# Optimization experiments

Hardware: AMD Instinct MI355X
Metric: run time of the kernel (lower is better)

## Reference

```python
import jax, jax.numpy as jnp
import numpy as np
from jax import lax

N_GROUPS = 128
EPS = 1e-5


def _instance_norm(x):
    # x: [B, C, H, W]; per-sample per-channel normalization over spatial dims
    mean = jnp.mean(x, axis=(2, 3), keepdims=True)
    var = jnp.mean(jnp.square(x - mean), axis=(2, 3), keepdims=True)
    return (x - mean) * lax.rsqrt(var + EPS)


def _reflect_pad(x, p):
    return jnp.pad(x, ((0, 0), (0, 0), (p, p), (p, p)), mode='reflect')


def _conv(x, w, groups):
    # x: [N, Cin, H, W], w: [Cout, Cin/groups, kh, kw], VALID padding
    return lax.conv_general_dilated(
        x, w, window_strides=(1, 1), padding='VALID',
        dimension_numbers=('NCHW', 'OIHW', 'NCHW'),
        feature_group_count=groups)


def _forward_single(xi, ws, wp, b):
    # xi: [1, C, H, W]; ws: [C_mid, C/G, k, k]; wp: [C_pw, C_mid/G, 1, 1]; b: [C_pw]
    k = ws.shape[-1]
    p = (k - 1) // 2  # k=3 -> ceil/floor both 1
    y = _conv(_reflect_pad(xi, p), ws, N_GROUPS)
    y = _conv(y, wp, N_GROUPS) + b[None, :, None, None]
    return y


def setup_inputs() -> dict:
    key = jax.random.key(0)
    ks = jax.random.split(key, 6)
    B, C, H, W = 4, 512, 128, 128
    x = jax.random.normal(ks[0], (B, C, H, W), dtype=jnp.float32)
    w_spatial = jax.random.normal(ks[1], (B, 512, 4, 3, 3), dtype=jnp.float32) * 0.05
    w_pointwise = jax.random.normal(ks[2], (B, 128, 4, 1, 1), dtype=jnp.float32) * 0.05
    bias = jax.random.normal(ks[3], (B, 128), dtype=jnp.float32) * 0.05
    conv_w = jax.random.normal(ks[4], (512, 512, 3, 3), dtype=jnp.float32) * 0.02
    conv_b = jax.random.normal(ks[5], (512,), dtype=jnp.float32) * 0.02
    return {"x": x, "w_spatial": w_spatial, "w_pointwise": w_pointwise,
            "bias": bias, "conv_w": conv_w, "conv_b": conv_b}


def reference(x, w_spatial, w_pointwise, bias, conv_w, conv_b):
    B, C, H, W = x.shape
    x = _instance_norm(x)
    # per-sample grouped spatial + pointwise conv, vmapped over batch
    ys = jax.vmap(_forward_single)(x[:, None], w_spatial, w_pointwise, bias)
    # ys: [B, 1, C_pw, H, W] -> concat along channel dim as in torch.cat(dim=1)
    ys = ys.reshape(1, B * ys.shape[2], H, W)
    # final standard conv, reflect padding (1,1), kernel 3
    out = _conv(_reflect_pad(ys, 1), conv_w, 1) + conv_b[None, :, None, None]
    return out
```

## Files before the change

### kernel.cpp

```cpp
#include <hip/hip_runtime.h>
#include <hip/hip_bf16.h>


typedef unsigned short u16;
typedef __attribute__((ext_vector_type(8))) short bf16x8;
typedef __attribute__((ext_vector_type(4))) float f32x4;

#define HW 16384
#define NBC 2048

__device__ __forceinline__ int refl(int i) {
    return i < 0 ? -i : (i > 127 ? 254 - i : i);
}

__device__ __forceinline__ u16 f2bf(float f) {
    union { float f; unsigned u; } x; x.f = f;
    unsigned r = x.u + 0x7fffu + ((x.u >> 16) & 1u);
    return (u16)(r >> 16);
}

__global__ __launch_bounds__(256) void stats_kernel(
        const float* __restrict__ x, float* __restrict__ mean,
        float* __restrict__ rstd) {
    int bc = blockIdx.x;
    const float4* p4 = (const float4*)(x + (size_t)bc * HW);
    float s = 0.f, ss = 0.f;
    for (int i = threadIdx.x; i < HW / 4; i += 256) {
        float4 v = p4[i];
        s  += v.x + v.y + v.z + v.w;
        ss += v.x * v.x + v.y * v.y + v.z * v.z + v.w * v.w;
    }
    for (int o = 32; o >= 1; o >>= 1) {
        s  += __shfl_down(s, o);
        ss += __shfl_down(ss, o);
    }
    __shared__ float sm[4], sm2[4];
    int wid = threadIdx.x >> 6, lane = threadIdx.x & 63;
    if (lane == 0) { sm[wid] = s; sm2[wid] = ss; }
    __syncthreads();
    if (threadIdx.x == 0) {
        float S = sm[0] + sm[1] + sm[2] + sm[3];
        float SS = sm2[0] + sm2[1] + sm2[2] + sm2[3];
        float m = S * (1.f / HW);
        float var = SS * (1.f / HW) - m * m;
        mean[bc] = m;
        rstd[bc] = rsqrtf(var + 1e-5f);
    }
}

__global__ __launch_bounds__(256) void weff_kernel(
        const float* __restrict__ wsp, const float* __restrict__ wpw,
        float* __restrict__ we) {
    int idx = blockIdx.x * 256 + threadIdx.x;
    if (idx >= 4 * 128 * 4 * 9) return;
    int k = idx % 9;
    int c = (idx / 9) & 3;
    int g = (idx / 36) & 127;
    int b = idx / 4608;
    float acc = 0.f;
#pragma unroll
    for (int m = 0; m < 4; ++m) {
        acc += wpw[(b * 128 + g) * 4 + m] *
               wsp[(((size_t)b * 512 + g * 4 + m) * 4 + c) * 9 + k];
    }
    we[idx] = acc;
}

__global__ __launch_bounds__(256) void midconv_kernel(
        const float* __restrict__ x, const float* __restrict__ mean,
        const float* __restrict__ rstd, const float* __restrict__ we,
        const float* __restrict__ bias, float* __restrict__ ys) {
    int bg = blockIdx.z;
    int b = bg >> 7, g = bg & 127;
    int x0 = blockIdx.x * 16, y0 = blockIdx.y * 16;
    __shared__ float tile[4][18][18];
    int t = threadIdx.x;
    for (int idx = t; idx < 4 * 18 * 18; idx += 256) {
        int c = idx / 324;
        int rem = idx - c * 324;
        int r = rem / 18, col = rem - r * 18;
        int ch = (b << 9) + (g << 2) + c;
        int gh = refl(y0 + r - 1), gw = refl(x0 + col - 1);
        float m = mean[ch], rs = rstd[ch];
        tile[c][r][col] = (x[((size_t)ch << 14) + (gh << 7) + gw] - m) * rs;
    }
    __syncthreads();
    int lx = t & 15, ly = t >> 4;
    const float* w = we + (size_t)bg * 36;
    float acc = bias[bg];
#pragma unroll
    for (int c = 0; c < 4; ++c)
#pragma unroll
        for (int kh = 0; kh < 3; ++kh)
#pragma unroll
            for (int kw = 0; kw < 3; ++kw)
                acc += w[c * 9 + kh * 3 + kw] * tile[c][ly + kh][lx + kw];
    ys[((size_t)bg << 14) + ((size_t)(y0 + ly) << 7) + (x0 + lx)] = acc;
}

__global__ __launch_bounds__(256) void transpose_ys(
        const float* __restrict__ ys, u16* __restrict__ ysT) {
    __shared__ u16 tile[64][72];
    int t = threadIdx.x;
    int pix0 = blockIdx.x * 64, ci0 = blockIdx.y * 64;
    for (int i = t; i < 64 * 16; i += 256) {
        int ci = i >> 4, px = (i & 15) * 4;
        float4 v = *(const float4*)&ys[(size_t)(ci0 + ci) * HW + pix0 + px];
        tile[ci][px + 0] = f2bf(v.x);
        tile[ci][px + 1] = f2bf(v.y);
        tile[ci][px + 2] = f2bf(v.z);
        tile[ci][px + 3] = f2bf(v.w);
    }
    __syncthreads();
    for (int i = t; i < 512; i += 256) {
        int px = i >> 3, c8 = i & 7;
        bf16x8 v;
#pragma unroll
        for (int j = 0; j < 8; ++j) v[j] = (short)tile[c8 * 8 + j][px];
        *(bf16x8*)&ysT[(size_t)(pix0 + px) * 512 + ci0 + c8 * 8] = v;
    }
}

__global__ __launch_bounds__(256) void wpack_kernel(
        const float* __restrict__ cw, u16* __restrict__ wT) {
    int idx = blockIdx.x * 256 + threadIdx.x;
    if (idx >= 9 * 512 * 512) return;
    int ci = idx & 511;
    int co = (idx >> 9) & 511;
    int tap = idx >> 18;
    wT[idx] = f2bf(cw[(size_t)co * 4608 + ci * 9 + tap]);
}

__device__ __forceinline__ void load_lds16(const u16* g, u16* l) {
    __builtin_amdgcn_global_load_lds(
        (const __attribute__((address_space(1))) unsigned int*)g,
        (__attribute__((address_space(3))) unsigned int*)l, 16, 0, 0);
}

__global__ __launch_bounds__(256, 2) void finalconv_mfma(
        const u16* __restrict__ ysT, const u16* __restrict__ wT,
        const float* __restrict__ cb, float* __restrict__ out) {
    __shared__ u16 lds_ys[528 * 32];
    __shared__ u16 lds_wt[576 * 32];
    int t = threadIdx.x;
    int w = t >> 6, l = t & 63;
    int m = l & 15, q = l >> 4;
    int co0 = blockIdx.x * 64;
    int y0 = blockIdx.y * 2;
    int tr = w >> 1, xw = (w & 1) * 64;

    f32x4 acc[4][4];
#pragma unroll
    for (int i = 0; i < 4; ++i)
#pragma unroll
        for (int j = 0; j < 4; ++j) acc[i][j] = (f32x4){0.f, 0.f, 0.f, 0.f};

    for (int ci0 = 0; ci0 < 512; ci0 += 32) {
        __syncthreads();
        for (int i = w; i < 69; i += 4) {
            if (i < 33) {
                int s = i * 64 + l;
                int p = s >> 2, c = s & 3;
                int pc = p > 519 ? 519 : p;
                int hr = (pc * 1009) >> 17;
                int hc = pc - hr * 130;
                int gy = refl(y0 + hr - 1), gx = refl(hc - 1);
                int ci8 = c ^ ((p >> 1) & 3);
                const u16* src = ysT + (size_t)((gy << 7) + gx) * 512 + ci0 + ci8 * 8;
                load_lds16(src, &lds_ys[i * 512]);
            } else {
                int k = i - 33;
                int s = k * 64 + l;
                int row = s >> 2, c = s & 3;
                int tap = row >> 6, co_l = row & 63;
                int ci8 = c ^ ((co_l >> 1) & 3);
                const u16* src = wT + (size_t)((tap << 9) + co0 + co_l) * 512 + ci0 + ci8 * 8;
                load_lds16(src, &lds_wt[k * 512]);
            }
        }
        __syncthreads();
#pragma unroll
        for (int tap = 0; tap < 9; ++tap) {
            const int dyi = tap / 3, dxi = tap % 3;
            bf16x8 a[4], b[4];
#pragma unroll
            for (int i = 0; i < 4; ++i) {
                int co_l = i * 16 + m;
                int ch = q ^ ((co_l >> 1) & 3);
                a[i] = *(const bf16x8*)&lds_wt[(tap * 64 + co_l) * 32 + ch * 8];
            }
#pragma unroll
            for (int j = 0; j < 4; ++j) {
                int xx = xw + j * 16 + m;
                int p = (tr + dyi) * 130 + xx + dxi;
                int ch = q ^ ((p >> 1) & 3);
                b[j] = *(const bf16x8*)&lds_ys[p * 32 + ch * 8];
            }
#pragma unroll
            for (int i = 0; i < 4; ++i)
#pragma unroll
                for (int j = 0; j < 4; ++j)
                    acc[i][j] = __builtin_amdgcn_mfma_f32_16x16x32_bf16(
                        a[i], b[j], acc[i][j], 0, 0, 0);
        }
    }
    int gyo = y0 + tr;
#pragma unroll
    for (int i = 0; i < 4; ++i) {
        int cob = co0 + i * 16 + q * 4;
#pragma unroll
        for (int j = 0; j < 4; ++j) {
            int xx = xw + j * 16 + m;
            float* o = out + (size_t)cob * HW + (gyo << 7) + xx;
#pragma unroll
            for (int r = 0; r < 4; ++r)
                o[(size_t)r * HW] = acc[i][j][r] + cb[cob + r];
        }
    }
}

extern "C" void kernel_launch(void* const* d_in, const int* in_sizes, int n_in,
                              void* d_out, int out_size, void* d_ws, size_t ws_size,
                              hipStream_t stream) {
    const float* x    = (const float*)d_in[0];
    const float* wsp  = (const float*)d_in[1];
    const float* wpw  = (const float*)d_in[2];
    const float* bias = (const float*)d_in[3];
    const float* cw   = (const float*)d_in[4];
    const float* cb   = (const float*)d_in[5];
    float* out = (float*)d_out;

    char* ws = (char*)d_ws;
    float* ys   = (float*)ws;
    u16*   ysT  = (u16*)(ws + 33554432);
    u16*   wT   = (u16*)(ws + 33554432 + 16777216);
    float* mean = (float*)(ws + 55050240);
    float* rstd = (float*)(ws + 55058432);
    float* we   = (float*)(ws + 55066624);

    stats_kernel<<<NBC, 256, 0, stream>>>(x, mean, rstd);
    weff_kernel<<<(4 * 128 * 4 * 9 + 255) / 256, 256, 0, stream>>>(wsp, wpw, we);
    wpack_kernel<<<(9 * 512 * 512 + 255) / 256, 256, 0, stream>>>(cw, wT);
    midconv_kernel<<<dim3(8, 8, 512), 256, 0, stream>>>(x, mean, rstd, we, bias, ys);
    transpose_ys<<<dim3(256, 8), 256, 0, stream>>>(ys, ysT);
    finalconv_mfma<<<dim3(8, 64), 256, 0, stream>>>(ysT, wT, cb, out);
}
```

Before: 375.7 us.

## Fuse mid grouped conv with bf16 transpose and coalesce weight packing

```diff
diff --git a/kernel.cpp b/kernel.cpp
--- a/kernel.cpp
+++ b/kernel.cpp
@@ -17,6 +17,18 @@
     union { float f; unsigned u; } x; x.f = f;
     unsigned r = x.u + 0x7fffu + ((x.u >> 16) & 1u);
     return (u16)(r >> 16);
+}
+
+__device__ __forceinline__ void load_lds16(const u16* g, u16* l) {
+    __builtin_amdgcn_global_load_lds(
+        (const __attribute__((address_space(1))) unsigned int*)g,
+        (__attribute__((address_space(3))) unsigned int*)l, 16, 0, 0);
+}
+
+__device__ __forceinline__ void load_lds4(const float* g, float* l) {
+    __builtin_amdgcn_global_load_lds(
+        (const __attribute__((address_space(1))) unsigned int*)g,
+        (__attribute__((address_space(3))) unsigned int*)l, 4, 0, 0);
 }
 
 __global__ __launch_bounds__(256) void stats_kernel(
@@ -66,75 +78,120 @@
     we[idx] = acc;
 }
 
-__global__ __launch_bounds__(256) void midconv_kernel(
+__global__ __launch_bounds__(256) void wpack_kernel(
+        const float* __restrict__ cw, u16* __restrict__ wT) {
+    __shared__ float s[512 * 10];
+    int t = threadIdx.x, co = blockIdx.x;
+    const float* src = cw + (size_t)co * 4608;
+    for (int i = t; i < 4608; i += 256) {
+        int ci = i / 9, tap = i - ci * 9;
+        s[ci * 10 + tap] = src[i];
+    }
+    __syncthreads();
+#pragma unroll
+    for (int tap = 0; tap < 9; ++tap) {
+        unsigned lo = (unsigned)f2bf(s[(2 * t) * 10 + tap]);
+        unsigned hi = (unsigned)f2bf(s[(2 * t + 1) * 10 + tap]);
+        ((unsigned*)&wT[((size_t)(tap << 9) + co) * 512])[t] = lo | (hi << 16);
+    }
+}
+
+__global__ __launch_bounds__(512) void midconv_fused(
         const float* __restrict__ x, const float* __restrict__ mean,
         const float* __restrict__ rstd, const float* __restrict__ we,
-        const float* __restrict__ bias, float* __restrict__ ys) {
-    int bg = blockIdx.z;
-    int b = bg >> 7, g = bg & 127;
-    int x0 = blockIdx.x * 16, y0 = blockIdx.y * 16;
-    __shared__ float tile[4][18][18];
+        const float* __restrict__ bias, u16* __restrict__ ysT) {
+    __shared__ float tile[16 * 324];
+    __shared__ u16 outb[256 * 72];
+    __shared__ float s_mean[512], s_rstd[512];
+    __shared__ float s_w[144];
+    __shared__ float s_bias[4];
     int t = threadIdx.x;
-    for (int idx = t; idx < 4 * 18 * 18; idx += 256) {
-        int c = idx / 324;
-        int rem = idx - c * 324;
-        int r = rem / 18, col = rem - r * 18;
-        int ch = (b << 9) + (g << 2) + c;
-        int gh = refl(y0 + r - 1), gw = refl(x0 + col - 1);
-        float m = mean[ch], rs = rstd[ch];
-        tile[c][r][col] = (x[((size_t)ch << 14) + (gh << 7) + gw] - m) * rs;
+    int b = blockIdx.y;
+    int x0 = (blockIdx.x & 7) << 4, y0 = (blockIdx.x >> 3) << 4;
+
+    s_mean[t] = mean[(b << 9) + t];
+    s_rstd[t] = rstd[(b << 9) + t];
+
+    int soff[11];
+#pragma unroll
+    for (int s = 0; s < 11; ++s) {
+        int idx = t + (s << 9);
+        int id2 = idx < 5184 ? idx : 0;
+        int c8 = id2 / 324;
+        int rm = id2 - c8 * 324;
+        int r = rm / 18, col = rm - r * 18;
+        soff[s] = (c8 << 14) + (refl(y0 + r - 1) << 7) + refl(x0 + col - 1);
+    }
+
+    int gq = t >> 7;
+    int rem = t & 127;
+    int py = rem >> 3;
+    int px0 = (rem & 7) << 1;
+    const float* wq = &s_w[gq * 36];
+
+    for (int q_i = 0; q_i < 32; ++q_i) {
+        __syncthreads();
+        if (q_i == 16) {
+            for (int i = t; i < 2048; i += 512) {
+                int pix = i >> 3, seg = i & 7;
+                bf16x8 v = *(const bf16x8*)&outb[pix * 72 + (seg << 3)];
+                int ppy = pix >> 4, ppx = pix & 15;
+                size_t gp = (size_t)(((y0 + ppy) << 7) + x0 + ppx);
+                *(bf16x8*)&ysT[gp * 512 + (b << 7) + (seg << 3)] = v;
+            }
+        }
+        const float* xq = x + ((size_t)((b << 9) + (q_i << 4)) << 14);
+#pragma unroll
+        for (int s = 0; s < 10; ++s)
+            load_lds4(xq + soff[s], &tile[t + (s << 9)]);
+        if (t < 64) load_lds4(xq + soff[10], &tile[t + 5120]);
+        if (t < 144) {
+            int g_rel = t / 36, rr = t - g_rel * 36;
+            int c = rr / 9;
+            int group = (q_i << 2) + g_rel;
+            s_w[t] = we[((b << 7) + group) * 36 + rr] *
+                     s_rstd[(group << 2) + c];
+        }
+        if (t < 4) {
+            int group = (q_i << 2) + t;
+            float bsum = bias[(b << 7) + group];
+            const float* wrow = we + ((b << 7) + group) * 36;
+#pragma unroll
+            for (int j = 0; j < 36; ++j) {
+                int ch_l = (group << 2) + (j / 9);
+                bsum -= wrow[j] * s_rstd[ch_l] * s_mean[ch_l];
+            }
+            s_bias[t] = bsum;
+        }
+        __syncthreads();
+        float a0 = s_bias[gq], a1 = a0;
+#pragma unroll
+        for (int c = 0; c < 4; ++c) {
+            const float* tp = &tile[(gq * 4 + c) * 324];
+#pragma unroll
+            for (int kh = 0; kh < 3; ++kh) {
+                float2 u = *(const float2*)&tp[(py + kh) * 18 + px0];
+                float2 v = *(const float2*)&tp[(py + kh) * 18 + px0 + 2];
+                float w0 = wq[c * 9 + kh * 3 + 0];
+                float w1 = wq[c * 9 + kh * 3 + 1];
+                float w2 = wq[c * 9 + kh * 3 + 2];
+                a0 += w0 * u.x + w1 * u.y + w2 * v.x;
+                a1 += w0 * u.y + w1 * v.x + w2 * v.y;
+            }
+        }
+        int col = ((q_i << 2) + gq) & 63;
+        int pix = (py << 4) + px0;
+        outb[pix * 72 + col] = f2bf(a0);
+        outb[(pix + 1) * 72 + col] = f2bf(a1);
     }
     __syncthreads();
-    int lx = t & 15, ly = t >> 4;
-    const float* w = we + (size_t)bg * 36;
-    float acc = bias[bg];
-#pragma unroll
-    for (int c = 0; c < 4; ++c)
-#pragma unroll
-        for (int kh = 0; kh < 3; ++kh)
-#pragma unroll
-            for (int kw = 0; kw < 3; ++kw)
-                acc += w[c * 9 + kh * 3 + kw] * tile[c][ly + kh][lx + kw];
-    ys[((size_t)bg << 14) + ((size_t)(y0 + ly) << 7) + (x0 + lx)] = acc;
-}
-
-__global__ __launch_bounds__(256) void transpose_ys(
-        const float* __restrict__ ys, u16* __restrict__ ysT) {
-    __shared__ u16 tile[64][72];
-    int t = threadIdx.x;
-    int pix0 = blockIdx.x * 64, ci0 = blockIdx.y * 64;
-    for (int i = t; i < 64 * 16; i += 256) {
-        int ci = i >> 4, px = (i & 15) * 4;
-        float4 v = *(const float4*)&ys[(size_t)(ci0 + ci) * HW + pix0 + px];
-        tile[ci][px + 0] = f2bf(v.x);
-        tile[ci][px + 1] = f2bf(v.y);
-        tile[ci][px + 2] = f2bf(v.z);
-        tile[ci][px + 3] = f2bf(v.w);
-    }
-    __syncthreads();
-    for (int i = t; i < 512; i += 256) {
-        int px = i >> 3, c8 = i & 7;
-        bf16x8 v;
-#pragma unroll
-        for (int j = 0; j < 8; ++j) v[j] = (short)tile[c8 * 8 + j][px];
-        *(bf16x8*)&ysT[(size_t)(pix0 + px) * 512 + ci0 + c8 * 8] = v;
-    }
-}
-
-__global__ __launch_bounds__(256) void wpack_kernel(
-        const float* __restrict__ cw, u16* __restrict__ wT) {
-    int idx = blockIdx.x * 256 + threadIdx.x;
-    if (idx >= 9 * 512 * 512) return;
-    int ci = idx & 511;
-    int co = (idx >> 9) & 511;
-    int tap = idx >> 18;
-    wT[idx] = f2bf(cw[(size_t)co * 4608 + ci * 9 + tap]);
-}
-
-__device__ __forceinline__ void load_lds16(const u16* g, u16* l) {
-    __builtin_amdgcn_global_load_lds(
-        (const __attribute__((address_space(1))) unsigned int*)g,
-        (__attribute__((address_space(3))) unsigned int*)l, 16, 0, 0);
+    for (int i = t; i < 2048; i += 512) {
+        int pix = i >> 3, seg = i & 7;
+        bf16x8 v = *(const bf16x8*)&outb[pix * 72 + (seg << 3)];
+        int ppy = pix >> 4, ppx = pix & 15;
+        size_t gp = (size_t)(((y0 + ppy) << 7) + x0 + ppx);
+        *(bf16x8*)&ysT[gp * 512 + (b << 7) + 64 + (seg << 3)] = v;
+    }
 }
 
 __global__ __launch_bounds__(256, 2) void finalconv_mfma(
@@ -145,8 +202,10 @@
     int t = threadIdx.x;
     int w = t >> 6, l = t & 63;
     int m = l & 15, q = l >> 4;
-    int co0 = blockIdx.x * 64;
-    int y0 = blockIdx.y * 2;
+    int bid = blockIdx.x;
+    int swz = ((bid & 7) << 6) + (bid >> 3);
+    int co0 = (swz & 7) << 6;
+    int y0 = (swz >> 3) << 1;
     int tr = w >> 1, xw = (w & 1) * 64;
 
     f32x4 acc[4][4];
@@ -231,17 +290,15 @@
     float* out = (float*)d_out;
 
     char* ws = (char*)d_ws;
-    float* ys   = (float*)ws;
-    u16*   ysT  = (u16*)(ws + 33554432);
-    u16*   wT   = (u16*)(ws + 33554432 + 16777216);
-    float* mean = (float*)(ws + 55050240);
-    float* rstd = (float*)(ws + 55058432);
-    float* we   = (float*)(ws + 55066624);
+    u16*   ysT  = (u16*)ws;
+    u16*   wT   = (u16*)(ws + 16777216);
+    float* mean = (float*)(ws + 21495808);
+    float* rstd = (float*)(ws + 21504000);
+    float* we   = (float*)(ws + 21512192);
 
     stats_kernel<<<NBC, 256, 0, stream>>>(x, mean, rstd);
     weff_kernel<<<(4 * 128 * 4 * 9 + 255) / 256, 256, 0, stream>>>(wsp, wpw, we);
-    wpack_kernel<<<(9 * 512 * 512 + 255) / 256, 256, 0, stream>>>(cw, wT);
-    midconv_kernel<<<dim3(8, 8, 512), 256, 0, stream>>>(x, mean, rstd, we, bias, ys);
-    transpose_ys<<<dim3(256, 8), 256, 0, stream>>>(ys, ysT);
-    finalconv_mfma<<<dim3(8, 64), 256, 0, stream>>>(ysT, wT, cb, out);
-}
+    wpack_kernel<<<512, 256, 0, stream>>>(cw, wT);
+    midconv_fused<<<dim3(64, 4), 512, 0, stream>>>(x, mean, rstd, we, bias, ysT);
+    finalconv_mfma<<<512, 256, 0, stream>>>(ysT, wT, cb, out);
+}
```

New measurement: 372.8 us. Within noise of the previous version (-0.8%).
